# Kernel optimization log

Hardware: AMD Instinct MI355X
Metric: run time of the kernel (lower is better)

Reference implementation:

```python
import jax, jax.numpy as jnp
import numpy as np

N = 50000      # nodes
E = 800000     # edges
DIN = 128      # input feature dim
H = 4          # heads
D = 16         # per-head output dim
NEG_SLOPE = 0.2


def setup_inputs() -> dict:
    key = jax.random.key(0)
    k1, k2, k3, k4, k5, k6 = jax.random.split(key, 6)
    h = jax.random.normal(k1, (N, DIN), dtype=jnp.float32)
    W = jax.random.normal(k2, (DIN, H * D), dtype=jnp.float32) * 0.05
    attn_l = jax.random.normal(k3, (H, D), dtype=jnp.float32) * 0.1
    attn_r = jax.random.normal(k4, (H, D), dtype=jnp.float32) * 0.1
    src = jax.random.randint(k5, (E,), 0, N, dtype=jnp.int32)
    dst = jax.random.randint(k6, (E,), 0, N, dtype=jnp.int32)
    return {"h": h, "W": W, "attn_l": attn_l, "attn_r": attn_r, "src": src, "dst": dst}


def reference(h, W, attn_l, attn_r, src, dst):
    n = h.shape[0]
    # linear projection: [N, H, D]
    feat = (h @ W).reshape(n, H, D)
    # per-node attention halves: [N, H]
    el = jnp.einsum('nhd,hd->nh', feat, attn_l)
    er = jnp.einsum('nhd,hd->nh', feat, attn_r)
    # per-edge logits: [E, H]
    e = jax.nn.leaky_relu(el[src] + er[dst], negative_slope=NEG_SLOPE)
    # segment softmax grouped by destination node
    m = jax.ops.segment_max(e, dst, num_segments=n)          # [N, H]
    ex = jnp.exp(e - m[dst])                                  # [E, H]
    denom = jax.ops.segment_sum(ex, dst, num_segments=n)     # [N, H]
    a = ex / denom[dst]                                       # [E, H]
    # weighted aggregation of source features: [E, H, D] -> [N, H, D]
    msg = a[:, :, None] * feat[src]
    out = jax.ops.segment_sum(msg, dst, num_segments=n)
    # mean over heads (the wrapper's .mean(1)): [N, D]
    return out.mean(axis=1)
```

## Files before the change

### kernel.cpp

```cpp
#include <hip/hip_runtime.h>
#include <hip/hip_fp16.h>

#define NN   50000
#define EE   800000
#define KDIN 128
#define NH   4
#define ND   16
#define NEG_SLOPE 0.2f

#define NB        196
#define CAP       5120
#define NNODE_PAD (NB * 256)

__device__ __forceinline__ float lrelu(float x) {
    return x > 0.f ? x : NEG_SLOPE * x;
}
__device__ __forceinline__ float h2f(unsigned short u) {
    return __half2float(__ushort_as_half(u));
}

__global__ __launch_bounds__(256) void k_proj(
    const float* __restrict__ h, const float* __restrict__ W,
    const float* __restrict__ attn_l, const float* __restrict__ attn_r,
    unsigned short* __restrict__ feat_h, float* __restrict__ el, float* __restrict__ er,
    int* __restrict__ gcur)
{
    __shared__ float4 Wl[KDIN * 16];
    __shared__ float  hrow[16 * 132];

    const int tid = threadIdx.x;
    if (blockIdx.x == 0) gcur[tid] = 0;

    const float4* W4 = (const float4*)W;
    #pragma unroll
    for (int i = 0; i < 8; ++i) Wl[tid + 256 * i] = W4[tid + 256 * i];

    const int wave = tid >> 6;
    const int lane = tid & 63;
    const int r16  = lane >> 4;
    const int c4   = lane & 15;
    const int row_base = blockIdx.x * 16 + wave * 4;

    {
        const float4* h4 = (const float4*)h;
        float4 v0 = h4[(size_t)row_base * 32 + lane];
        float4 v1 = h4[(size_t)row_base * 32 + lane + 64];
        const int i1 = lane + 64;
        *(float4*)&hrow[(wave * 4 + (lane >> 5)) * 132 + (lane & 31) * 4] = v0;
        *(float4*)&hrow[(wave * 4 + (i1  >> 5)) * 132 + (i1  & 31) * 4] = v1;
    }
    __syncthreads();

    const float* myrow = &hrow[(wave * 4 + r16) * 132];
    float4 acc = make_float4(0.f, 0.f, 0.f, 0.f);
    #pragma unroll 8
    for (int k = 0; k < KDIN; ++k) {
        float  hv = myrow[k];
        float4 w  = Wl[k * 16 + c4];
        acc.x = fmaf(hv, w.x, acc.x);
        acc.y = fmaf(hv, w.y, acc.y);
        acc.z = fmaf(hv, w.z, acc.z);
        acc.w = fmaf(hv, w.w, acc.w);
    }
    const int row = row_base + r16;

    ushort4 hv4;
    hv4.x = __half_as_ushort(__float2half_rn(acc.x));
    hv4.y = __half_as_ushort(__float2half_rn(acc.y));
    hv4.z = __half_as_ushort(__float2half_rn(acc.z));
    hv4.w = __half_as_ushort(__float2half_rn(acc.w));
    ((ushort4*)feat_h)[(size_t)row * 16 + c4] = hv4;

    const float4 al = ((const float4*)attn_l)[c4];
    const float4 ar = ((const float4*)attn_r)[c4];
    float pl = acc.x*al.x + acc.y*al.y + acc.z*al.z + acc.w*al.w;
    float pr = acc.x*ar.x + acc.y*ar.y + acc.z*ar.z + acc.w*ar.w;
    pl += __shfl_xor(pl, 1); pl += __shfl_xor(pl, 2);
    pr += __shfl_xor(pr, 1); pr += __shfl_xor(pr, 2);
    if ((c4 & 3) == 0) {
        const int head = c4 >> 2;
        el[row * NH + head] = pl;
        er[row * NH + head] = pr;
    }
}

__global__ __launch_bounds__(256) void k_part(
    const int* __restrict__ src, const int* __restrict__ dst,
    int* __restrict__ gcur, int2* __restrict__ pairs)
{
    __shared__ int lhist[NB];
    const int tid = threadIdx.x;
    const int eb  = blockIdx.x * 1280;

    int dreg[5], sreg[5];
    if (tid < NB) lhist[tid] = 0;
    __syncthreads();

    #pragma unroll
    for (int j = 0; j < 5; ++j) {
        const int e = eb + j * 256 + tid;
        dreg[j] = dst[e];
        sreg[j] = src[e];
        atomicAdd(&lhist[dreg[j] >> 8], 1);
    }
    __syncthreads();

    if (tid < NB) lhist[tid] = atomicAdd(&gcur[tid], lhist[tid]);
    __syncthreads();

    #pragma unroll
    for (int j = 0; j < 5; ++j) {
        const int b   = dreg[j] >> 8;
        const int idx = atomicAdd(&lhist[b], 1);
        if (idx < CAP) pairs[b * CAP + idx] = make_int2(sreg[j], dreg[j]);
    }
}

__global__ __launch_bounds__(256) void k_lsort(
    const int* __restrict__ gcur, const int2* __restrict__ pairs,
    int* __restrict__ sorted_src, int* __restrict__ row_start, int* __restrict__ degv)
{
    __shared__ int lhist[256];
    __shared__ int lpre[256];
    const int tid = threadIdx.x;
    const int b   = blockIdx.x;
    const int n   = min(gcur[b], CAP);

    lhist[tid] = 0;
    __syncthreads();

    for (int i = tid; i < n; i += 256)
        atomicAdd(&lhist[pairs[b * CAP + i].y & 255], 1);
    __syncthreads();

    if (tid == 0) {
        int run = 0;
        for (int i = 0; i < 256; ++i) { lpre[i] = run; run += lhist[i]; }
    }
    __syncthreads();

    const int node = b * 256 + tid;
    row_start[node] = b * CAP + lpre[tid];
    degv[node]      = lhist[tid];
    lhist[tid] = lpre[tid];
    __syncthreads();

    for (int i = tid; i < n; i += 256) {
        const int2 p = pairs[b * CAP + i];
        const int  r = atomicAdd(&lhist[p.y & 255], 1);
        sorted_src[b * CAP + r] = p.x;
    }
}

__global__ __launch_bounds__(256) void k_gather(
    const float* __restrict__ el, const float* __restrict__ er,
    const unsigned short* __restrict__ feat_h,
    const int* __restrict__ sorted_src,
    const int* __restrict__ row_start, const int* __restrict__ degv,
    float* __restrict__ out)
{
    const int tid = threadIdx.x;
    const int t   = blockIdx.x * 4 + (tid >> 6);
    if (t >= NN) return;
    const int lane = tid & 63;
    const int hd   = lane >> 4;
    const int base = row_start[t];
    const int n    = degv[t];
    const float er_h = er[t * NH + hd];

    float acc = 0.f, dsum = 0.f;
    int j = 0;
    for (; j + 4 <= n; j += 4) {
        const int s0 = sorted_src[base + j + 0];
        const int s1 = sorted_src[base + j + 1];
        const int s2 = sorted_src[base + j + 2];
        const int s3 = sorted_src[base + j + 3];
        const float x0 = el[s0 * NH + hd] + er_h;
        const float x1 = el[s1 * NH + hd] + er_h;
        const float x2 = el[s2 * NH + hd] + er_h;
        const float x3 = el[s3 * NH + hd] + er_h;
        const float f0 = h2f(feat_h[(size_t)s0 * 64 + lane]);
        const float f1 = h2f(feat_h[(size_t)s1 * 64 + lane]);
        const float f2 = h2f(feat_h[(size_t)s2 * 64 + lane]);
        const float f3 = h2f(feat_h[(size_t)s3 * 64 + lane]);
        const float e0 = __expf(lrelu(x0));
        const float e1 = __expf(lrelu(x1));
        const float e2 = __expf(lrelu(x2));
        const float e3 = __expf(lrelu(x3));
        dsum += (e0 + e1) + (e2 + e3);
        acc = fmaf(e0, f0, acc);
        acc = fmaf(e1, f1, acc);
        acc = fmaf(e2, f2, acc);
        acc = fmaf(e3, f3, acc);
    }
    for (; j < n; ++j) {
        const int s = sorted_src[base + j];
        const float x  = el[s * NH + hd] + er_h;
        const float fv = h2f(feat_h[(size_t)s * 64 + lane]);
        const float ex = __expf(lrelu(x));
        dsum += ex;
        acc = fmaf(ex, fv, acc);
    }

    float r = (n > 0) ? acc * __builtin_amdgcn_rcpf(dsum) : 0.f;
    r += __shfl_xor(r, 16);
    r += __shfl_xor(r, 32);
    if (lane < 16) out[t * ND + lane] = 0.25f * r;
}

extern "C" void kernel_launch(void* const* d_in, const int* in_sizes, int n_in,
                              void* d_out, int out_size, void* d_ws, size_t ws_size,
                              hipStream_t stream)
{
    const float* h  = (const float*)d_in[0];
    const float* W  = (const float*)d_in[1];
    const float* al = (const float*)d_in[2];
    const float* ar = (const float*)d_in[3];
    const int* src  = (const int*)d_in[4];
    const int* dst  = (const int*)d_in[5];
    float* out = (float*)d_out;

    unsigned short* feat_h = (unsigned short*)d_ws;
    float* el   = (float*)(feat_h + (size_t)NN * 64);
    float* er   = el + (size_t)NN * NH;
    int*   gcur = (int*)(er + (size_t)NN * NH);
    int2*  pairs = (int2*)(gcur + 256);
    int*   ssrc  = (int*)(pairs + (size_t)NB * CAP);
    int*   row_start = ssrc + (size_t)NB * CAP;
    int*   degv      = row_start + NNODE_PAD;

    k_proj  <<<NN / 16,   256, 0, stream>>>(h, W, al, ar, feat_h, el, er, gcur);
    k_part  <<<EE / 1280, 256, 0, stream>>>(src, dst, gcur, pairs);
    k_lsort <<<NB,        256, 0, stream>>>(gcur, pairs, ssrc, row_start, degv);
    k_gather<<<NN / 4,    256, 0, stream>>>(el, er, feat_h, ssrc, row_start, degv, out);
}
```

Before: 162.2 us.

## Pack edge pairs to 32 bits, 16-bit sorted indices, 2-row projection, LDS-staged sort

Each edge's (src, dst low byte) pair is packed into one 32-bit word, and the sorted source indices are stored as 16-bit values, which is valid because N < 65536. This cuts memory traffic in the partition, sort and gather kernels. The local sort now runs 512 threads, stages the bucket in shared memory to avoid a second global read, and uses a parallel prefix scan instead of a single-thread serial scan. The projection kernel computes two rows per thread to reuse each W load from LDS, with bounds guards added for the padded last block. The packed formats rely on the node count fitting in 16 bits.

```diff
diff --git a/kernel.cpp b/kernel.cpp
--- a/kernel.cpp
+++ b/kernel.cpp
@@ -11,6 +11,8 @@
 #define NB        196
 #define CAP       5120
 #define NNODE_PAD (NB * 256)
+#define PROJ_ROWS 32
+#define PROJ_LDP  130
 
 __device__ __forceinline__ float lrelu(float x) {
     return x > 0.f ? x : NEG_SLOPE * x;
@@ -26,7 +28,7 @@
     int* __restrict__ gcur)
 {
     __shared__ float4 Wl[KDIN * 16];
-    __shared__ float  hrow[16 * 132];
+    __shared__ float  hrow[PROJ_ROWS * PROJ_LDP];
 
     const int tid = threadIdx.x;
     if (blockIdx.x == 0) gcur[tid] = 0;
@@ -35,73 +37,98 @@
     #pragma unroll
     for (int i = 0; i < 8; ++i) Wl[tid + 256 * i] = W4[tid + 256 * i];
 
-    const int wave = tid >> 6;
-    const int lane = tid & 63;
-    const int r16  = lane >> 4;
-    const int c4   = lane & 15;
-    const int row_base = blockIdx.x * 16 + wave * 4;
+    const int row_base = blockIdx.x * PROJ_ROWS;
 
     {
         const float4* h4 = (const float4*)h;
-        float4 v0 = h4[(size_t)row_base * 32 + lane];
-        float4 v1 = h4[(size_t)row_base * 32 + lane + 64];
-        const int i1 = lane + 64;
-        *(float4*)&hrow[(wave * 4 + (lane >> 5)) * 132 + (lane & 31) * 4] = v0;
-        *(float4*)&hrow[(wave * 4 + (i1  >> 5)) * 132 + (i1  & 31) * 4] = v1;
-    }
-    __syncthreads();
-
-    const float* myrow = &hrow[(wave * 4 + r16) * 132];
-    float4 acc = make_float4(0.f, 0.f, 0.f, 0.f);
+        #pragma unroll
+        for (int i = 0; i < 4; ++i) {
+            const int idx = tid + 256 * i;
+            const int r   = idx >> 5;
+            const int c   = idx & 31;
+            int gr = row_base + r;
+            if (gr >= NN) gr = NN - 1;
+            float4 v = h4[(size_t)gr * 32 + c];
+            *(float4*)&hrow[r * PROJ_LDP + c * 4] = v;
+        }
+    }
+    __syncthreads();
+
+    const int c4 = tid & 15;
+    const int rg = tid >> 4;
+    const float* row0 = &hrow[(rg * 2    ) * PROJ_LDP];
+    const float* row1 = &hrow[(rg * 2 + 1) * PROJ_LDP];
+
+    float4 a0 = make_float4(0.f, 0.f, 0.f, 0.f);
+    float4 a1 = make_float4(0.f, 0.f, 0.f, 0.f);
     #pragma unroll 8
     for (int k = 0; k < KDIN; ++k) {
-        float  hv = myrow[k];
-        float4 w  = Wl[k * 16 + c4];
-        acc.x = fmaf(hv, w.x, acc.x);
-        acc.y = fmaf(hv, w.y, acc.y);
-        acc.z = fmaf(hv, w.z, acc.z);
-        acc.w = fmaf(hv, w.w, acc.w);
-    }
-    const int row = row_base + r16;
-
-    ushort4 hv4;
-    hv4.x = __half_as_ushort(__float2half_rn(acc.x));
-    hv4.y = __half_as_ushort(__float2half_rn(acc.y));
-    hv4.z = __half_as_ushort(__float2half_rn(acc.z));
-    hv4.w = __half_as_ushort(__float2half_rn(acc.w));
-    ((ushort4*)feat_h)[(size_t)row * 16 + c4] = hv4;
+        const float4 w  = Wl[k * 16 + c4];
+        const float  h0 = row0[k];
+        const float  h1 = row1[k];
+        a0.x = fmaf(h0, w.x, a0.x);
+        a0.y = fmaf(h0, w.y, a0.y);
+        a0.z = fmaf(h0, w.z, a0.z);
+        a0.w = fmaf(h0, w.w, a0.w);
+        a1.x = fmaf(h1, w.x, a1.x);
+        a1.y = fmaf(h1, w.y, a1.y);
+        a1.z = fmaf(h1, w.z, a1.z);
+        a1.w = fmaf(h1, w.w, a1.w);
+    }
+
+    const int r0 = row_base + rg * 2;
+    const int r1 = r0 + 1;
+
+    ushort4 v0, v1;
+    v0.x = __half_as_ushort(__float2half_rn(a0.x));
+    v0.y = __half_as_ushort(__float2half_rn(a0.y));
+    v0.z = __half_as_ushort(__float2half_rn(a0.z));
+    v0.w = __half_as_ushort(__float2half_rn(a0.w));
+    v1.x = __half_as_ushort(__float2half_rn(a1.x));
+    v1.y = __half_as_ushort(__float2half_rn(a1.y));
+    v1.z = __half_as_ushort(__float2half_rn(a1.z));
+    v1.w = __half_as_ushort(__float2half_rn(a1.w));
+    if (r0 < NN) ((ushort4*)feat_h)[(size_t)r0 * 16 + c4] = v0;
+    if (r1 < NN) ((ushort4*)feat_h)[(size_t)r1 * 16 + c4] = v1;
 
     const float4 al = ((const float4*)attn_l)[c4];
     const float4 ar = ((const float4*)attn_r)[c4];
-    float pl = acc.x*al.x + acc.y*al.y + acc.z*al.z + acc.w*al.w;
-    float pr = acc.x*ar.x + acc.y*ar.y + acc.z*ar.z + acc.w*ar.w;
-    pl += __shfl_xor(pl, 1); pl += __shfl_xor(pl, 2);
-    pr += __shfl_xor(pr, 1); pr += __shfl_xor(pr, 2);
+    float pl0 = a0.x*al.x + a0.y*al.y + a0.z*al.z + a0.w*al.w;
+    float pr0 = a0.x*ar.x + a0.y*ar.y + a0.z*ar.z + a0.w*ar.w;
+    float pl1 = a1.x*al.x + a1.y*al.y + a1.z*al.z + a1.w*al.w;
+    float pr1 = a1.x*ar.x + a1.y*ar.y + a1.z*ar.z + a1.w*ar.w;
+    pl0 += __shfl_xor(pl0, 1); pl0 += __shfl_xor(pl0, 2);
+    pr0 += __shfl_xor(pr0, 1); pr0 += __shfl_xor(pr0, 2);
+    pl1 += __shfl_xor(pl1, 1); pl1 += __shfl_xor(pl1, 2);
+    pr1 += __shfl_xor(pr1, 1); pr1 += __shfl_xor(pr1, 2);
     if ((c4 & 3) == 0) {
         const int head = c4 >> 2;
-        el[row * NH + head] = pl;
-        er[row * NH + head] = pr;
+        if (r0 < NN) { el[r0 * NH + head] = pl0; er[r0 * NH + head] = pr0; }
+        if (r1 < NN) { el[r1 * NH + head] = pl1; er[r1 * NH + head] = pr1; }
     }
 }
 
 __global__ __launch_bounds__(256) void k_part(
     const int* __restrict__ src, const int* __restrict__ dst,
-    int* __restrict__ gcur, int2* __restrict__ pairs)
+    int* __restrict__ gcur, unsigned int* __restrict__ pairs)
 {
     __shared__ int lhist[NB];
     const int tid = threadIdx.x;
     const int eb  = blockIdx.x * 1280;
 
-    int dreg[5], sreg[5];
+    unsigned int preg[5];
+    int breg[5];
     if (tid < NB) lhist[tid] = 0;
     __syncthreads();
 
     #pragma unroll
     for (int j = 0; j < 5; ++j) {
         const int e = eb + j * 256 + tid;
-        dreg[j] = dst[e];
-        sreg[j] = src[e];
-        atomicAdd(&lhist[dreg[j] >> 8], 1);
+        const int d = dst[e];
+        const int s = src[e];
+        breg[j] = d >> 8;
+        preg[j] = (unsigned int)s | ((unsigned int)(d & 255) << 16);
+        atomicAdd(&lhist[breg[j]], 1);
     }
     __syncthreads();
 
@@ -110,52 +137,65 @@
 
     #pragma unroll
     for (int j = 0; j < 5; ++j) {
-        const int b   = dreg[j] >> 8;
+        const int b   = breg[j];
         const int idx = atomicAdd(&lhist[b], 1);
-        if (idx < CAP) pairs[b * CAP + idx] = make_int2(sreg[j], dreg[j]);
-    }
-}
-
-__global__ __launch_bounds__(256) void k_lsort(
-    const int* __restrict__ gcur, const int2* __restrict__ pairs,
-    int* __restrict__ sorted_src, int* __restrict__ row_start, int* __restrict__ degv)
-{
+        if (idx < CAP) pairs[b * CAP + idx] = preg[j];
+    }
+}
+
+__global__ __launch_bounds__(512) void k_lsort(
+    const int* __restrict__ gcur, const unsigned int* __restrict__ pairs,
+    unsigned short* __restrict__ sorted_src,
+    int* __restrict__ row_start, int* __restrict__ degv)
+{
+    __shared__ unsigned int buf[CAP];
     __shared__ int lhist[256];
     __shared__ int lpre[256];
     const int tid = threadIdx.x;
     const int b   = blockIdx.x;
     const int n   = min(gcur[b], CAP);
 
-    lhist[tid] = 0;
-    __syncthreads();
-
-    for (int i = tid; i < n; i += 256)
-        atomicAdd(&lhist[pairs[b * CAP + i].y & 255], 1);
-    __syncthreads();
-
-    if (tid == 0) {
-        int run = 0;
-        for (int i = 0; i < 256; ++i) { lpre[i] = run; run += lhist[i]; }
-    }
-    __syncthreads();
-
-    const int node = b * 256 + tid;
-    row_start[node] = b * CAP + lpre[tid];
-    degv[node]      = lhist[tid];
-    lhist[tid] = lpre[tid];
-    __syncthreads();
-
-    for (int i = tid; i < n; i += 256) {
-        const int2 p = pairs[b * CAP + i];
-        const int  r = atomicAdd(&lhist[p.y & 255], 1);
-        sorted_src[b * CAP + r] = p.x;
+    if (tid < 256) lhist[tid] = 0;
+    __syncthreads();
+
+    for (int i = tid; i < n; i += 512) {
+        const unsigned int p = pairs[b * CAP + i];
+        buf[i] = p;
+        atomicAdd(&lhist[(p >> 16) & 255], 1);
+    }
+    __syncthreads();
+
+    if (tid < 256) lpre[tid] = lhist[tid];
+    __syncthreads();
+    #pragma unroll
+    for (int off = 1; off < 256; off <<= 1) {
+        int v = 0;
+        if (tid < 256 && tid >= off) v = lpre[tid - off];
+        __syncthreads();
+        if (tid < 256) lpre[tid] += v;
+        __syncthreads();
+    }
+
+    if (tid < 256) {
+        const int node = b * 256 + tid;
+        const int excl = lpre[tid] - lhist[tid];
+        row_start[node] = b * CAP + excl;
+        degv[node]      = lhist[tid];
+        lhist[tid]      = excl;
+    }
+    __syncthreads();
+
+    for (int i = tid; i < n; i += 512) {
+        const unsigned int p = buf[i];
+        const int r = atomicAdd(&lhist[(p >> 16) & 255], 1);
+        sorted_src[b * CAP + r] = (unsigned short)(p & 0xFFFFu);
     }
 }
 
 __global__ __launch_bounds__(256) void k_gather(
     const float* __restrict__ el, const float* __restrict__ er,
     const unsigned short* __restrict__ feat_h,
-    const int* __restrict__ sorted_src,
+    const unsigned short* __restrict__ sorted_src,
     const int* __restrict__ row_start, const int* __restrict__ degv,
     float* __restrict__ out)
 {
@@ -171,10 +211,10 @@
     float acc = 0.f, dsum = 0.f;
     int j = 0;
     for (; j + 4 <= n; j += 4) {
-        const int s0 = sorted_src[base + j + 0];
-        const int s1 = sorted_src[base + j + 1];
-        const int s2 = sorted_src[base + j + 2];
-        const int s3 = sorted_src[base + j + 3];
+        const int s0 = (int)sorted_src[base + j + 0];
+        const int s1 = (int)sorted_src[base + j + 1];
+        const int s2 = (int)sorted_src[base + j + 2];
+        const int s3 = (int)sorted_src[base + j + 3];
         const float x0 = el[s0 * NH + hd] + er_h;
         const float x1 = el[s1 * NH + hd] + er_h;
         const float x2 = el[s2 * NH + hd] + er_h;
@@ -194,7 +234,7 @@
         acc = fmaf(e3, f3, acc);
     }
     for (; j < n; ++j) {
-        const int s = sorted_src[base + j];
+        const int s = (int)sorted_src[base + j];
         const float x  = el[s * NH + hd] + er_h;
         const float fv = h2f(feat_h[(size_t)s * 64 + lane]);
         const float ex = __expf(lrelu(x));
@@ -224,13 +264,14 @@
     float* el   = (float*)(feat_h + (size_t)NN * 64);
     float* er   = el + (size_t)NN * NH;
     int*   gcur = (int*)(er + (size_t)NN * NH);
-    int2*  pairs = (int2*)(gcur + 256);
-    int*   ssrc  = (int*)(pairs + (size_t)NB * CAP);
-    int*   row_start = ssrc + (size_t)NB * CAP;
+    unsigned int* pairs = (unsigned int*)(gcur + 256);
+    unsigned short* ssrc = (unsigned short*)(pairs + (size_t)NB * CAP);
+    int*   row_start = (int*)(ssrc + (size_t)NB * CAP);
     int*   degv      = row_start + NNODE_PAD;
 
-    k_proj  <<<NN / 16,   256, 0, stream>>>(h, W, al, ar, feat_h, el, er, gcur);
-    k_part  <<<EE / 1280, 256, 0, stream>>>(src, dst, gcur, pairs);
-    k_lsort <<<NB,        256, 0, stream>>>(gcur, pairs, ssrc, row_start, degv);
-    k_gather<<<NN / 4,    256, 0, stream>>>(el, er, feat_h, ssrc, row_start, degv, out);
-}
+    const int proj_blocks = (NN + PROJ_ROWS - 1) / PROJ_ROWS;
+    k_proj  <<<proj_blocks, 256, 0, stream>>>(h, W, al, ar, feat_h, el, er, gcur);
+    k_part  <<<EE / 1280,   256, 0, stream>>>(src, dst, gcur, pairs);
+    k_lsort <<<NB,          512, 0, stream>>>(gcur, pairs, ssrc, row_start, degv);
+    k_gather<<<NN / 4,      256, 0, stream>>>(el, er, feat_h, ssrc, row_start, degv, out);
+}
```

Result: faster. 153.5 us (-5.4%).
